# Optimization experiments

Hardware: AMD Instinct MI355X
Metric: run time of the kernel (lower is better)

Reference implementation:

```python
import jax, jax.numpy as jnp
import numpy as np

DIM = 2048
H = 16          # n_heads
HKV = 4         # n_kv_heads
NREP = H // HKV
ROPE_D = 64
NOPE_D = 128
V_D = 128
QK_D = ROPE_D + NOPE_D
KV_RANK = 512
Q_RANK = 1536
B, T = 2, 2048


def _rope_cache(seq_len, head_dim, dtype=jnp.float32):
    # theta over even dims, angles concatenated [ang, ang] -> [T, head_dim]
    theta = 1.0 / (10000.0 ** (jnp.arange(0, head_dim, 2, dtype=dtype) / head_dim))
    pos = jnp.arange(seq_len, dtype=dtype)
    ang = jnp.outer(pos, theta)
    ang = jnp.concatenate([ang, ang], axis=-1)
    return jnp.cos(ang), jnp.sin(ang)  # each [T, head_dim]


def _rotate_half(x):
    half = x.shape[-1] // 2
    return jnp.concatenate([-x[..., half:], x[..., :half]], axis=-1)


def _apply_rope(x, cos, sin):
    # x: [B, T, h, d]; cos/sin: [T, d] broadcast over batch and heads
    return x * cos[None, :, None, :] + _rotate_half(x) * sin[None, :, None, :]


def setup_inputs() -> dict:
    key = jax.random.key(0)
    ks = jax.random.split(key, 9)
    s = 0.02
    return {
        "x": jax.random.normal(ks[0], (B, T, DIM), jnp.float32),
        "W_kv_down": jax.random.normal(ks[1], (DIM, KV_RANK), jnp.float32) * s,
        "W_k_nope": jax.random.normal(ks[2], (KV_RANK, HKV * NOPE_D), jnp.float32) * s,
        "W_k_rope": jax.random.normal(ks[3], (KV_RANK, HKV * ROPE_D), jnp.float32) * s,
        "W_v": jax.random.normal(ks[4], (KV_RANK, HKV * V_D), jnp.float32) * s,
        "W_q_down": jax.random.normal(ks[5], (DIM, Q_RANK), jnp.float32) * s,
        "W_q_nope": jax.random.normal(ks[6], (Q_RANK, H * NOPE_D), jnp.float32) * s,
        "W_q_rope": jax.random.normal(ks[7], (Q_RANK, H * ROPE_D), jnp.float32) * s,
        "W_o": jax.random.normal(ks[8], (H * V_D, DIM), jnp.float32) * s,
    }


def reference(x, W_kv_down, W_k_nope, W_k_rope, W_v, W_q_down, W_q_nope, W_q_rope, W_o):
    Bx, Tx, _ = x.shape
    scale = 1.0 / np.sqrt(QK_D)

    kv_c = x @ W_kv_down                                        # [B,T,KV_RANK]
    k_nope = (kv_c @ W_k_nope).reshape(Bx, Tx, HKV, NOPE_D)
    k_rope = (kv_c @ W_k_rope).reshape(Bx, Tx, HKV, ROPE_D)
    v = (kv_c @ W_v).reshape(Bx, Tx, HKV, V_D)

    q_c = x @ W_q_down                                          # [B,T,Q_RANK]
    q_nope = (q_c @ W_q_nope).reshape(Bx, Tx, H, NOPE_D)
    q_rope = (q_c @ W_q_rope).reshape(Bx, Tx, H, ROPE_D)

    cos, sin = _rope_cache(Tx, ROPE_D, x.dtype)
    q_rope = _apply_rope(q_rope, cos, sin)
    k_rope = _apply_rope(k_rope, cos, sin)

    q = jnp.concatenate([q_nope, q_rope], axis=-1).transpose(0, 2, 1, 3)  # [B,H,T,QK_D]
    k = jnp.concatenate([k_nope, k_rope], axis=-1).transpose(0, 2, 1, 3)  # [B,HKV,T,QK_D]
    vh = v.transpose(0, 2, 1, 3)                                          # [B,HKV,T,V_D]

    k = jnp.repeat(k, NREP, axis=1)   # GQA repeat -> [B,H,T,QK_D]
    vh = jnp.repeat(vh, NREP, axis=1)

    attn = jnp.einsum("bhqd,bhkd->bhqk", q, k) * scale
    causal = jnp.triu(jnp.ones((Tx, Tx), dtype=bool), k=1)
    attn = jnp.where(causal[None, None], -jnp.inf, attn)
    attn = jax.nn.softmax(attn, axis=-1)

    out = jnp.einsum("bhqk,bhkd->bhqd", attn, vh)               # [B,H,T,V_D]
    out = out.transpose(0, 2, 1, 3).reshape(Bx, Tx, H * V_D)
    return out @ W_o
```

## Files before the change

### kernel.cpp

```cpp
#include <hip/hip_runtime.h>
#include <hip/hip_bf16.h>

typedef __bf16 bf16;
typedef __attribute__((ext_vector_type(8))) __bf16 bf16x8;
typedef __attribute__((ext_vector_type(4))) __bf16 bf16x4;
typedef __attribute__((ext_vector_type(2))) __bf16 bf16x2;
typedef __attribute__((ext_vector_type(4))) float f32x4;

#define NH 16
#define NKV 4
#define ROPE_DIM 64
#define NOPE_DIM 128
#define V_DIM 128
#define QK_DIM 192
#define TT 2048
#define BB 2
#define MM 4096

#define QK_SCALE 0.07216878364870323f

__device__ __forceinline__ void gload16(const bf16* g, bf16* l) {
    __builtin_amdgcn_global_load_lds(
        (const __attribute__((address_space(1))) void*)g,
        (__attribute__((address_space(3))) void*)l, 16, 0, 0);
}

struct PrepArgs {
    const float* wsrc[8];
    bf16* wdst[8];
    const float* x;
    bf16* xb;
    float* ct;
    float* st;
};

__global__ __launch_bounds__(256) void k_prep(PrepArgs a) {
    constexpr int WR[8] = {2048, 2048, 512, 512, 512, 1536, 1536, 2048};
    constexpr int WC[8] = {512, 1536, 512, 256, 512, 2048, 1024, 2048};
    const int bid = blockIdx.x;
    if (bid < 13440) {
        int w = 0, base = 0;
        #pragma unroll
        for (int i = 0; i < 8; i++) {
            int t = (WC[i] >> 5) * (WR[i] >> 5);
            if (w == i && bid >= base + t) { base += t; w = i + 1; }
        }
        const int local = bid - base;
        const int R = WR[w], C = WC[w];
        const int tilesX = C >> 5;
        const int tyt = local / tilesX, txt = local - tyt * tilesX;
        const int c0 = txt * 32, r0 = tyt * 32;
        const float* s = a.wsrc[w];
        bf16* d = a.wdst[w];
        __shared__ float tile[32][33];
        int tx = threadIdx.x & 31, ty = threadIdx.x >> 5;
        #pragma unroll
        for (int rr = ty; rr < 32; rr += 8)
            tile[rr][tx] = s[(size_t)(r0 + rr) * C + c0 + tx];
        __syncthreads();
        #pragma unroll
        for (int q = threadIdx.x; q < 512; q += 256) {
            int ccq = q >> 4, pr = (q & 15) << 1;
            bf16x2 v;
            v[0] = (bf16)tile[pr][ccq];
            v[1] = (bf16)tile[pr + 1][ccq];
            *(bf16x2*)&d[(size_t)(c0 + ccq) * R + r0 + pr] = v;
        }
    } else if (bid < 13696) {
        int idx = (bid - 13440) * 256 + threadIdx.x;
        int t = idx >> 5, i = idx & 31;
        float theta = powf(10000.f, -(float)(2 * i) / 64.f);
        float ang = (float)t * theta;
        a.ct[idx] = cosf(ang);
        a.st[idx] = sinf(ang);
    } else {
        int i = (bid - 13696) * 256 + threadIdx.x;
        float4 v = *(const float4*)(a.x + (size_t)i * 4);
        bf16* o = a.xb + (size_t)i * 4;
        o[0] = (bf16)v.x; o[1] = (bf16)v.y; o[2] = (bf16)v.z; o[3] = (bf16)v.w;
    }
}

template<int EPI>
__global__ __launch_bounds__(256) void k_gemm(const bf16* __restrict__ A, int lda,
                                              const bf16* __restrict__ Bt, int ldb,
                                              void* __restrict__ Cv, int ldc, int K,
                                              const float* __restrict__ ct,
                                              const float* __restrict__ st,
                                              bf16* __restrict__ vt) {
    __shared__ __align__(16) bf16 As[2][128 * 32];
    __shared__ __align__(16) bf16 Bs[2][128 * 32];
    const int tid = threadIdx.x;
    const int lane = tid & 63;
    const int wid = tid >> 6;
    const int wr = wid >> 1, wc = wid & 1;
    const int g = lane >> 4, c = lane & 15;
    const int m0 = blockIdx.y * 128, n0 = blockIdx.x * 128;

    f32x4 acc[4][4] = {};
    const int rdswz = (g ^ ((c >> 1) & 3)) * 8;

    auto stage = [&](int buf, int k0) {
        #pragma unroll
        for (int i = 0; i < 2; i++) {
            int ch = tid + 256 * i;
            int row = ch >> 2;
            int kc = (ch & 3) ^ ((ch >> 3) & 3);
            gload16(A + (size_t)(m0 + row) * lda + k0 + kc * 8, &As[buf][ch * 8]);
            gload16(Bt + (size_t)(n0 + row) * ldb + k0 + kc * 8, &Bs[buf][ch * 8]);
        }
    };

    stage(0, 0);
    __syncthreads();
    const int nt = K >> 5;
    for (int t = 0; t < nt; ++t) {
        const int cur = t & 1;
        if (t + 1 < nt) stage(cur ^ 1, (t + 1) << 5);
        bf16x8 af[4], bfr[4];
        #pragma unroll
        for (int i = 0; i < 4; i++)
            af[i] = *(const bf16x8*)&As[cur][(wr * 64 + i * 16 + c) * 32 + rdswz];
        #pragma unroll
        for (int j = 0; j < 4; j++)
            bfr[j] = *(const bf16x8*)&Bs[cur][(wc * 64 + j * 16 + c) * 32 + rdswz];
        #pragma unroll
        for (int i = 0; i < 4; i++)
            #pragma unroll
            for (int j = 0; j < 4; j++)
                acc[i][j] = __builtin_amdgcn_mfma_f32_16x16x32_bf16(
                    af[i], bfr[j], acc[i][j], 0, 0, 0);
        __syncthreads();
    }

    if constexpr (EPI <= 1) {
        #pragma unroll
        for (int i = 0; i < 4; i++) {
            int row = m0 + wr * 64 + i * 16 + g * 4;
            #pragma unroll
            for (int j = 0; j < 4; j++) {
                int col = n0 + wc * 64 + j * 16 + c;
                #pragma unroll
                for (int r = 0; r < 4; r++) {
                    if (EPI == 1)
                        ((float*)Cv)[(size_t)(row + r) * ldc + col] = acc[i][j][r];
                    else
                        ((bf16*)Cv)[(size_t)(row + r) * ldc + col] = (bf16)acc[i][j][r];
                }
            }
        }
    } else if constexpr (EPI == 2) {
        bf16* ka = (bf16*)Cv;
        #pragma unroll
        for (int i = 0; i < 4; i++) {
            int row = m0 + wr * 64 + i * 16 + g * 4;
            int bq = row >> 11, t0 = row & 2047;
            #pragma unroll
            for (int j = 0; j < 4; j++) {
                int col = n0 + wc * 64 + j * 16 + c;
                if (col < 512) {
                    int h = col >> 7, d = col & 127;
                    bf16* dst = ka + ((size_t)(bq * NKV + h) * TT + t0) * QK_DIM + d;
                    #pragma unroll
                    for (int r = 0; r < 4; r++) dst[r * QK_DIM] = (bf16)acc[i][j][r];
                } else if (col < 768) {
                    int cr = col - 512;
                    int h = cr >> 6, dr = cr & 63, ia = dr & 31;
                    float sgn = (dr < 32) ? -1.f : 1.f;
                    bf16* dst = ka + ((size_t)(bq * NKV + h) * TT + t0) * QK_DIM + 128 + dr;
                    #pragma unroll
                    for (int r = 0; r < 4; r++) {
                        float cs = ct[(t0 + r) * 32 + ia], sn = st[(t0 + r) * 32 + ia];
                        dst[r * QK_DIM] = (bf16)(acc[i][j][r] * cs + sgn * acc[i][j ^ 2][r] * sn);
                    }
                } else {
                    int cr = col - 768;
                    int h = cr >> 7, d = cr & 127;
                    bf16x4 pk;
                    #pragma unroll
                    for (int r = 0; r < 4; r++) pk[r] = (bf16)acc[i][j][r];
                    *(bf16x4*)&vt[((size_t)((bq * NKV + h) * V_DIM + d)) * TT + t0] = pk;
                }
            }
        }
    } else {
        bf16* qa = (bf16*)Cv;
        #pragma unroll
        for (int i = 0; i < 4; i++) {
            int row = m0 + wr * 64 + i * 16 + g * 4;
            int bq = row >> 11, t0 = row & 2047;
            #pragma unroll
            for (int j = 0; j < 4; j++) {
                int col = n0 + wc * 64 + j * 16 + c;
                if (col < 2048) {
                    int h = col >> 7, d = col & 127;
                    bf16* dst = qa + ((size_t)(bq * NH + h) * TT + t0) * QK_DIM + d;
                    #pragma unroll
                    for (int r = 0; r < 4; r++)
                        dst[r * QK_DIM] = (bf16)(acc[i][j][r] * QK_SCALE);
                } else {
                    int cr = col - 2048;
                    int h = cr >> 6, dr = cr & 63, ia = dr & 31;
                    float sgn = (dr < 32) ? -1.f : 1.f;
                    bf16* dst = qa + ((size_t)(bq * NH + h) * TT + t0) * QK_DIM + 128 + dr;
                    #pragma unroll
                    for (int r = 0; r < 4; r++) {
                        float cs = ct[(t0 + r) * 32 + ia], sn = st[(t0 + r) * 32 + ia];
                        dst[r * QK_DIM] =
                            (bf16)((acc[i][j][r] * cs + sgn * acc[i][j ^ 2][r] * sn) * QK_SCALE);
                    }
                }
            }
        }
    }
}

__global__ __launch_bounds__(256, 2) void k_attn(const bf16* __restrict__ qa,
                                                 const bf16* __restrict__ ka,
                                                 const bf16* __restrict__ vt,
                                                 bf16* __restrict__ out) {
    __shared__ __align__(16) bf16 Klds[64 * QK_DIM];
    __shared__ __align__(16) bf16 Vlds[128 * 64];
    __shared__ __align__(16) bf16 Plds[4][32 * 64];

    const int tid  = threadIdx.x;
    const int lane = tid & 63;
    const int wid  = tid >> 6;
    const int g = lane >> 4, c = lane & 15;
    const int hsw = c & 7;

    const int qi = (blockIdx.y & 16) ? (15 - (int)blockIdx.x) : (int)blockIdx.x;
    const int q0 = qi * 128;
    const int bh = blockIdx.y;
    const int b = bh >> 4, h = bh & 15;
    const int kv = b * NKV + (h >> 2);
    const int qb0 = q0 + wid * 32;

    bf16x8 qf[2][6];
    #pragma unroll
    for (int qs = 0; qs < 2; ++qs) {
        const bf16* qp = qa + ((size_t)bh * TT + qb0 + qs * 16 + c) * QK_DIM + g * 8;
        #pragma unroll
        for (int cc = 0; cc < 6; ++cc) qf[qs][cc] = *(const bf16x8*)(qp + cc * 32);
    }

    f32x4 accO[2][8] = {};
    float l[2] = {0.f, 0.f};

    const bf16* kbase = ka + (size_t)kv * TT * QK_DIM;
    const bf16* vbase = vt + (size_t)kv * V_DIM * TT;

    const int nk = 2 * qi + 2;
    for (int it = 0; it < nk; ++it) {
        const int k0 = it * 64;
        __syncthreads();
        #pragma unroll
        for (int i = 0; i < 6; ++i) {
            int ch = tid + 256 * i;
            int row = ch / 24, cs = ch % 24;
            int gc = cs ^ (row & 7);
            gload16(kbase + (size_t)(k0 + row) * QK_DIM + gc * 8, &Klds[ch * 8]);
        }
        #pragma unroll
        for (int i = 0; i < 4; ++i) {
            int ch = tid + 256 * i;
            int row = ch >> 3, cs = ch & 7;
            int gc = cs ^ (row & 7);
            gload16(vbase + (size_t)row * TT + k0 + gc * 8, &Vlds[ch * 8]);
        }
        __syncthreads();

        if (k0 > qb0 + 15) continue;
        const bool a1 = (k0 <= qb0 + 31);

        f32x4 s[2][4] = {};
        #pragma unroll
        for (int cc = 0; cc < 6; ++cc) {
            #pragma unroll
            for (int j = 0; j < 4; ++j) {
                bf16x8 kf = *(const bf16x8*)&Klds[(j * 16 + c) * QK_DIM +
                                                  ((4 * cc + g) ^ hsw) * 8];
                s[0][j] = __builtin_amdgcn_mfma_f32_16x16x32_bf16(kf, qf[0][cc], s[0][j], 0, 0, 0);
                s[1][j] = __builtin_amdgcn_mfma_f32_16x16x32_bf16(kf, qf[1][cc], s[1][j], 0, 0, 0);
            }
        }

        #pragma unroll
        for (int qs = 0; qs < 2; ++qs) {
            if (qs == 1 && !a1) break;
            const int qb = qb0 + qs * 16;
            if (k0 + 63 > qb) {
                #pragma unroll
                for (int j = 0; j < 4; ++j)
                    #pragma unroll
                    for (int r = 0; r < 4; ++r)
                        if (k0 + j * 16 + g * 4 + r > qb + c) s[qs][j][r] = -1e30f;
            }
            float ps = 0.f;
            #pragma unroll
            for (int j = 0; j < 4; ++j) {
                bf16x4 pk;
                #pragma unroll
                for (int r = 0; r < 4; ++r) {
                    float e = __expf(s[qs][j][r]);
                    ps += e;
                    pk[r] = (bf16)e;
                }
                *(bf16x4*)&Plds[wid][(qs * 16 + c) * 64 +
                                     ((j * 16 + g * 4) ^ (hsw * 8))] = pk;
            }
            ps += __shfl_xor(ps, 16, 64);
            ps += __shfl_xor(ps, 32, 64);
            l[qs] += ps;
        }

        if (a1) {
            #pragma unroll
            for (int kc = 0; kc < 2; ++kc) {
                bf16x8 pf0 = *(const bf16x8*)&Plds[wid][(c)      * 64 + ((kc * 32 + g * 8) ^ (hsw * 8))];
                bf16x8 pf1 = *(const bf16x8*)&Plds[wid][(16 + c) * 64 + ((kc * 32 + g * 8) ^ (hsw * 8))];
                #pragma unroll
                for (int nj = 0; nj < 8; ++nj) {
                    bf16x8 vf = *(const bf16x8*)&Vlds[(nj * 16 + c) * 64 +
                                                      ((4 * kc + g) ^ hsw) * 8];
                    accO[0][nj] = __builtin_amdgcn_mfma_f32_16x16x32_bf16(vf, pf0, accO[0][nj], 0, 0, 0);
                    accO[1][nj] = __builtin_amdgcn_mfma_f32_16x16x32_bf16(vf, pf1, accO[1][nj], 0, 0, 0);
                }
            }
        } else {
            #pragma unroll
            for (int kc = 0; kc < 2; ++kc) {
                bf16x8 pf0 = *(const bf16x8*)&Plds[wid][(c) * 64 + ((kc * 32 + g * 8) ^ (hsw * 8))];
                #pragma unroll
                for (int nj = 0; nj < 8; ++nj) {
                    bf16x8 vf = *(const bf16x8*)&Vlds[(nj * 16 + c) * 64 +
                                                      ((4 * kc + g) ^ hsw) * 8];
                    accO[0][nj] = __builtin_amdgcn_mfma_f32_16x16x32_bf16(vf, pf0, accO[0][nj], 0, 0, 0);
                }
            }
        }
    }

    #pragma unroll
    for (int qs = 0; qs < 2; ++qs) {
        float inv = 1.f / l[qs];
        size_t rowoff = ((size_t)(b * TT + qb0 + qs * 16 + c)) * (NH * V_DIM) + h * V_DIM;
        #pragma unroll
        for (int nj = 0; nj < 8; ++nj) {
            bf16x4 o;
            #pragma unroll
            for (int r = 0; r < 4; ++r) o[r] = (bf16)(accO[qs][nj][r] * inv);
            *(bf16x4*)&out[rowoff + nj * 16 + g * 4] = o;
        }
    }
}

extern "C" void kernel_launch(void* const* d_in, const int* in_sizes, int n_in,
                              void* d_out, int out_size, void* d_ws, size_t ws_size,
                              hipStream_t stream) {
    const float* x    = (const float*)d_in[0];

    char* p = (char*)d_ws;
    size_t off = 0;
    auto take = [&](size_t elems, size_t esz) -> void* {
        void* r = p + off;
        off += ((elems * esz + 255) / 256) * 256;
        return r;
    };

    bf16* XB  = (bf16*)take((size_t)MM * 2048, 2);
    bf16* BT1 = (bf16*)take((size_t)2048 * 2048, 2);
    bf16* BT2 = (bf16*)take((size_t)1280 * 512, 2);
    bf16* BT3 = (bf16*)take((size_t)3072 * 1536, 2);
    bf16* BTO = (bf16*)take((size_t)2048 * 2048, 2);
    bf16* C1  = (bf16*)take((size_t)MM * 2048, 2);
    bf16* QA  = (bf16*)take((size_t)BB * NH * TT * QK_DIM, 2);
    bf16* KA  = (bf16*)take((size_t)BB * NKV * TT * QK_DIM, 2);
    bf16* VT  = (bf16*)take((size_t)BB * NKV * V_DIM * TT, 2);
    bf16* AO  = (bf16*)take((size_t)MM * 2048, 2);
    float* CT = (float*)take((size_t)TT * 32, 4);
    float* ST = (float*)take((size_t)TT * 32, 4);
    (void)ws_size; (void)in_sizes; (void)n_in; (void)out_size;

    PrepArgs pa;
    pa.wsrc[0] = (const float*)d_in[1]; pa.wdst[0] = BT1;
    pa.wsrc[1] = (const float*)d_in[5]; pa.wdst[1] = BT1 + (size_t)512 * 2048;
    pa.wsrc[2] = (const float*)d_in[2]; pa.wdst[2] = BT2;
    pa.wsrc[3] = (const float*)d_in[3]; pa.wdst[3] = BT2 + (size_t)512 * 512;
    pa.wsrc[4] = (const float*)d_in[4]; pa.wdst[4] = BT2 + (size_t)768 * 512;
    pa.wsrc[5] = (const float*)d_in[6]; pa.wdst[5] = BT3;
    pa.wsrc[6] = (const float*)d_in[7]; pa.wdst[6] = BT3 + (size_t)2048 * 1536;
    pa.wsrc[7] = (const float*)d_in[8]; pa.wdst[7] = BTO;
    pa.x = x; pa.xb = XB; pa.ct = CT; pa.st = ST;
    k_prep<<<21888, 256, 0, stream>>>(pa);

    k_gemm<0><<<dim3(16, 32), 256, 0, stream>>>(XB, 2048, BT1, 2048, C1, 2048, 2048,
                                                nullptr, nullptr, nullptr);
    k_gemm<2><<<dim3(10, 32), 256, 0, stream>>>(C1, 2048, BT2, 512, KA, 0, 512,
                                                CT, ST, VT);
    k_gemm<3><<<dim3(24, 32), 256, 0, stream>>>(C1 + 512, 2048, BT3, 1536, QA, 0, 1536,
                                                CT, ST, nullptr);

    k_attn<<<dim3(16, BB * NH), 256, 0, stream>>>(QA, KA, VT, AO);

    k_gemm<1><<<dim3(16, 32), 256, 0, stream>>>(AO, 2048, BTO, 2048, d_out, 2048, 2048,
                                                nullptr, nullptr, nullptr);
}
```

Baseline: 381.3 us.

## Merge KV and Q up-projection GEMMs into one launch with XCD-aware block swizzle

Grid launches for the GEMMs become 1D, and block IDs are remapped so that consecutive tiles land on the same XCD, which should improve L2 reuse of shared A/B panels. The KV up-projection (320 tiles) and Q up-projection (768 tiles) are fused into a single 1088-block kernel that dispatches by block id. This removes one launch and the tail gap between the two GEMMs, and lets both fill the GPU together. The swizzle assumes the block count is divisible by 8, which holds for 512 and 1088.

Result: slower. 392.8 us (+3.0%).

```diff
diff --git a/kernel.cpp b/kernel.cpp
--- a/kernel.cpp
+++ b/kernel.cpp
@@ -23,6 +23,11 @@
     __builtin_amdgcn_global_load_lds(
         (const __attribute__((address_space(1))) void*)g,
         (__attribute__((address_space(3))) void*)l, 16, 0, 0);
+}
+
+__device__ __forceinline__ int xcd_swz(int id, int nwg) {
+    int cpx = nwg >> 3;
+    return (id & 7) * cpx + (id >> 3);
 }
 
 struct PrepArgs {
@@ -82,20 +87,19 @@
 }
 
 template<int EPI>
-__global__ __launch_bounds__(256) void k_gemm(const bf16* __restrict__ A, int lda,
-                                              const bf16* __restrict__ Bt, int ldb,
-                                              void* __restrict__ Cv, int ldc, int K,
-                                              const float* __restrict__ ct,
-                                              const float* __restrict__ st,
-                                              bf16* __restrict__ vt) {
-    __shared__ __align__(16) bf16 As[2][128 * 32];
-    __shared__ __align__(16) bf16 Bs[2][128 * 32];
+__device__ __forceinline__ void gemm_body(
+        bf16 (*As)[128 * 32], bf16 (*Bs)[128 * 32], int bx, int by,
+        const bf16* __restrict__ A, int lda,
+        const bf16* __restrict__ Bt, int ldb,
+        void* __restrict__ Cv, int ldc, int K,
+        const float* __restrict__ ct, const float* __restrict__ st,
+        bf16* __restrict__ vt) {
     const int tid = threadIdx.x;
     const int lane = tid & 63;
     const int wid = tid >> 6;
     const int wr = wid >> 1, wc = wid & 1;
     const int g = lane >> 4, c = lane & 15;
-    const int m0 = blockIdx.y * 128, n0 = blockIdx.x * 128;
+    const int m0 = by * 128, n0 = bx * 128;
 
     f32x4 acc[4][4] = {};
     const int rdswz = (g ^ ((c >> 1) & 3)) * 8;
@@ -212,6 +216,40 @@
                 }
             }
         }
+    }
+}
+
+template<int EPI>
+__global__ __launch_bounds__(256) void k_gemm(const bf16* __restrict__ A, int lda,
+                                              const bf16* __restrict__ Bt, int ldb,
+                                              void* __restrict__ Cv, int ldc, int K,
+                                              const float* __restrict__ ct,
+                                              const float* __restrict__ st,
+                                              bf16* __restrict__ vt,
+                                              int nbx, int nwg) {
+    __shared__ __align__(16) bf16 As[2][128 * 32];
+    __shared__ __align__(16) bf16 Bs[2][128 * 32];
+    const int id = xcd_swz(blockIdx.x, nwg);
+    gemm_body<EPI>(As, Bs, id % nbx, id / nbx, A, lda, Bt, ldb, Cv, ldc, K, ct, st, vt);
+}
+
+__global__ __launch_bounds__(256) void k_gemm23(const bf16* __restrict__ C1,
+                                                const bf16* __restrict__ BT2,
+                                                const bf16* __restrict__ BT3,
+                                                bf16* __restrict__ KA,
+                                                bf16* __restrict__ QA,
+                                                bf16* __restrict__ VT,
+                                                const float* __restrict__ ct,
+                                                const float* __restrict__ st) {
+    __shared__ __align__(16) bf16 As[2][128 * 32];
+    __shared__ __align__(16) bf16 Bs[2][128 * 32];
+    const int id = xcd_swz(blockIdx.x, 1088);
+    if (id < 320) {
+        gemm_body<2>(As, Bs, id % 10, id / 10, C1, 2048, BT2, 512, KA, 0, 512, ct, st, VT);
+    } else {
+        const int b2 = id - 320;
+        gemm_body<3>(As, Bs, b2 % 24, b2 / 24, C1 + 512, 2048, BT3, 1536, QA, 0, 1536,
+                     ct, st, nullptr);
     }
 }
 
@@ -394,15 +432,12 @@
     pa.x = x; pa.xb = XB; pa.ct = CT; pa.st = ST;
     k_prep<<<21888, 256, 0, stream>>>(pa);
 
-    k_gemm<0><<<dim3(16, 32), 256, 0, stream>>>(XB, 2048, BT1, 2048, C1, 2048, 2048,
-                                                nullptr, nullptr, nullptr);
-    k_gemm<2><<<dim3(10, 32), 256, 0, stream>>>(C1, 2048, BT2, 512, KA, 0, 512,
-                                                CT, ST, VT);
-    k_gemm<3><<<dim3(24, 32), 256, 0, stream>>>(C1 + 512, 2048, BT3, 1536, QA, 0, 1536,
-                                                CT, ST, nullptr);
+    k_gemm<0><<<512, 256, 0, stream>>>(XB, 2048, BT1, 2048, C1, 2048, 2048,
+                                       nullptr, nullptr, nullptr, 16, 512);
+    k_gemm23<<<1088, 256, 0, stream>>>(C1, BT2, BT3, KA, QA, VT, CT, ST);
 
     k_attn<<<dim3(16, BB * NH), 256, 0, stream>>>(QA, KA, VT, AO);
 
-    k_gemm<1><<<dim3(16, 32), 256, 0, stream>>>(AO, 2048, BTO, 2048, d_out, 2048, 2048,
-                                                nullptr, nullptr, nullptr);
-}
+    k_gemm<1><<<512, 256, 0, stream>>>(AO, 2048, BTO, 2048, d_out, 2048, 2048,
+                                       nullptr, nullptr, nullptr, 16, 512);
+}
```
